# Kernel tuning notes

Hardware: AMD Instinct MI355X
Metric: run time of the kernel (lower is better)

Reference implementation:

```python
import jax, jax.numpy as jnp
import numpy as np

N_NODES = 10000
N_EDGES = 160000
F_DIM = 64
H = 4


def setup_inputs() -> dict:
    key = jax.random.key(0)
    ks = jax.random.split(key, 10)
    s = 1.0 / np.sqrt(F_DIM)  # xavier-ish scale
    return {
        "x": jax.random.normal(ks[0], (N_NODES, F_DIM), jnp.float32),
        "edge_index": jax.random.randint(ks[1], (2, N_EDGES), 0, N_NODES),
        "edge_vec": jax.random.normal(ks[2], (N_EDGES, 3), jnp.float32),
        "edge_len": jax.random.uniform(ks[3], (N_EDGES,), jnp.float32, 0.1, 5.0),
        "w_proj_W": jax.random.normal(ks[4], (H, F_DIM, F_DIM), jnp.float32) * s,
        "radial_W": jax.random.normal(ks[5], (H, F_DIM, F_DIM), jnp.float32) * s,
        "tangential_W": jax.random.normal(ks[6], (H, F_DIM, F_DIM), jnp.float32) * s,
        "radial_score": jax.random.normal(ks[7], (H, F_DIM), jnp.float32) * s,
        "tangential_score": jax.random.normal(ks[8], (H, F_DIM), jnp.float32) * s,
        "radial_distance_log_scale": jnp.zeros((), jnp.float32),
        "radial_temp_bias": jnp.zeros((H,), jnp.float32),
        "radial_temp_weight": jnp.zeros((H,), jnp.float32),
        "w_out_W": jax.random.normal(ks[9], (F_DIM, F_DIM), jnp.float32) * s,
    }


def _segment_softmax(logits, receiver, num_nodes):
    # logits: [E, H]; softmax over all edges sharing the same receiver.
    # Equivalent to the original's degree-bucketed per-group softmax.
    m = jax.ops.segment_max(logits, receiver, num_segments=num_nodes)  # [N, H]
    a = jnp.exp(logits - m[receiver])
    d = jax.ops.segment_sum(a, receiver, num_segments=num_nodes)       # [N, H]
    return a / d[receiver]


def reference(x, edge_index, edge_vec, edge_len, w_proj_W, radial_W, tangential_W,
              radial_score, tangential_score, radial_distance_log_scale,
              radial_temp_bias, radial_temp_weight, w_out_W):
    sender, receiver = edge_index[0], edge_index[1]
    n = x.shape[0]

    # Per-head bias-free linear projections (o3.Linear on scalar irreps).
    energy = jnp.einsum('nf,hfg->hng', x, w_proj_W)       # [H, N, F]
    radial = jnp.einsum('nf,hfg->hng', x, radial_W)       # [H, N, F]
    tang = jnp.einsum('nf,hfg->hng', x, tangential_W)     # [H, N, F]

    e_d = energy[:, sender] - energy[:, receiver]                       # [H, E, F]
    r_d = jnp.transpose(radial[:, sender] - radial[:, receiver], (1, 0, 2))  # [E, H, F]
    t_d = jnp.transpose(tang[:, sender] - tang[:, receiver], (1, 0, 2))      # [E, H, F]

    scale = jax.nn.softplus(radial_distance_log_scale)
    r_log = jnp.einsum('hef,hf->eh', e_d, radial_score) - scale * edge_len[:, None]  # [E, H]
    temp = jax.nn.softplus(radial_temp_bias[None, :] + radial_temp_weight[None, :] * edge_len[:, None])
    r_log = r_log / (temp + 0.0001)
    t_log = jnp.einsum('hef,hf->eh', e_d, tangential_score)                          # [E, H]

    r_alpha = _segment_softmax(r_log, receiver, n)  # [E, H]
    t_alpha = _segment_softmax(t_log, receiver, n)  # [E, H]

    r_msg = jax.ops.segment_sum(r_alpha[:, :, None] * r_d, receiver, num_segments=n)  # [N, H, F]
    t_msg = jax.ops.segment_sum(t_alpha[:, :, None] * t_d, receiver, num_segments=n)  # [N, H, F]

    out = jnp.nan_to_num((r_msg + t_msg).mean(axis=1))  # mean over heads -> [N, F]
    return x + out @ w_out_W
```

## Files before the change

kernel.cpp:

```cpp
#include <hip/hip_runtime.h>
#include <math.h>

#define N_NODES 10000
#define N_EDGES 160000
#define CAP 64

#define NB_SCORE 40
#define NB_BUCKET 625
#define NB_WPP 9
#define NB_D1 (NB_SCORE + NB_BUCKET + NB_WPP)

typedef short bf16x8 __attribute__((ext_vector_type(8)));
typedef float f32x4 __attribute__((ext_vector_type(4)));

__device__ __forceinline__ float bf2f(unsigned short u) {
    return __uint_as_float(((unsigned int)u) << 16);
}
__device__ __forceinline__ unsigned short f2bf(float f) {
    unsigned int x = __float_as_uint(f);
    unsigned int r = (x + 0x7fffu + ((x >> 16) & 1u)) >> 16;
    return (unsigned short)r;
}
__device__ __forceinline__ float softplus_f(float x) {
    return fmaxf(x, 0.f) + log1pf(expf(-fabsf(x)));
}

__global__ void __launch_bounds__(256) k_prep(const float* __restrict__ x,
                                              const float* __restrict__ wproj,
                                              const float* __restrict__ wrad,
                                              const float* __restrict__ wtan,
                                              const float* __restrict__ rsc,
                                              const float* __restrict__ tsc,
                                              const float* __restrict__ wout,
                                              const int* __restrict__ ei,
                                              const float* __restrict__ el,
                                              float* __restrict__ rs,
                                              float* __restrict__ ts,
                                              int* __restrict__ cur,
                                              int2* __restrict__ sbuf,
                                              unsigned short* __restrict__ wppT) {
    __shared__ __align__(16) float smem[8192];
    int b = blockIdx.x;
    int t = threadIdx.x;

    if (b < NB_SCORE) {
        float* vrl = smem;
        float* vtl = smem + 256;
        {
            int h = t >> 6, f = t & 63;
            const float* wrow = wproj + h * 4096 + f * 64;
            const float* rsp = rsc + h * 64;
            const float* tsp = tsc + h * 64;
            float ar = 0.f, at = 0.f;
            for (int g = 0; g < 64; ++g) {
                float w = wrow[g];
                ar += w * rsp[g];
                at += w * tsp[g];
            }
            vrl[t] = ar;
            vtl[t] = at;
        }
        __syncthreads();
        int n = b * 256 + t;
        if (n >= N_NODES) return;
        const float4* xr = (const float4*)(x + n * 64);
        float accr[4] = {0.f, 0.f, 0.f, 0.f};
        float acct[4] = {0.f, 0.f, 0.f, 0.f};
        for (int i = 0; i < 16; ++i) {
            float4 xv = xr[i];
#pragma unroll
            for (int h = 0; h < 4; ++h) {
                float4 a = ((const float4*)vrl)[h * 16 + i];
                accr[h] += xv.x * a.x + xv.y * a.y + xv.z * a.z + xv.w * a.w;
                float4 bb = ((const float4*)vtl)[h * 16 + i];
                acct[h] += xv.x * bb.x + xv.y * bb.y + xv.z * bb.z + xv.w * bb.w;
            }
        }
        ((float4*)rs)[n] = make_float4(accr[0], accr[1], accr[2], accr[3]);
        ((float4*)ts)[n] = make_float4(acct[0], acct[1], acct[2], acct[3]);
    } else if (b < NB_SCORE + NB_BUCKET) {
        int e = (b - NB_SCORE) * 256 + t;
        if (e >= N_EDGES) return;
        int s = ei[e];
        int r = ei[N_EDGES + e];
        float len = el[e];
        int pos = atomicAdd(&cur[r], 1);
        if (pos < CAP) sbuf[r * CAP + pos] = make_int2(s, __float_as_int(len));
    } else {
        int k = b - NB_SCORE - NB_BUCKET;
        float* wo = smem;
        float* am = smem + 4096;
        for (int i = 0; i < 16; ++i) wo[t + 256 * i] = wout[t + 256 * i];
        if (k < 8) {
            const float* M = (k < 4) ? (wrad + k * 4096) : (wtan + (k - 4) * 4096);
            for (int i = 0; i < 16; ++i) am[t + 256 * i] = M[t + 256 * i];
        } else {
            for (int i = 0; i < 16; ++i) {
                int e = t + 256 * i;
                float s = 0.f;
#pragma unroll
                for (int h = 0; h < 4; ++h) s += wrad[h * 4096 + e] + wtan[h * 4096 + e];
                am[e] = -s;
            }
        }
        __syncthreads();
        int c = t & 63;
        int fg = t >> 6;
        for (int j = 0; j < 16; ++j) {
            int f = fg * 16 + j;
            float acc = 0.f;
            for (int g = 0; g < 64; ++g) acc += am[f * 64 + g] * wo[g * 64 + c];
            wppT[c * 576 + k * 64 + f] = f2bf(acc * 0.25f);
        }
    }
}

__global__ void __launch_bounds__(256) k_node(const int* __restrict__ cur,
                                              const int2* __restrict__ sbuf,
                                              const float* __restrict__ rs,
                                              const float* __restrict__ ts,
                                              const float* __restrict__ rdls,
                                              const float* __restrict__ tb,
                                              const float* __restrict__ tw,
                                              const float* __restrict__ x,
                                              const unsigned short* __restrict__ wppT,
                                              float* __restrict__ out) {
    __shared__ __align__(16) unsigned short accL[16 * 584];
    __shared__ __align__(16) float aldsb[4][CAP * 8];
    __shared__ int sldsb[4][CAP];
    int t = threadIdx.x;
    int wid = t >> 6, lane = t & 63;
    int blk = blockIdx.x;

    float scale = softplus_f(rdls[0]);
    float tb0 = tb[0], tb1 = tb[1], tb2 = tb[2], tb3 = tb[3];
    float tw0 = tw[0], tw1 = tw[1], tw2 = tw[2], tw3 = tw[3];
    float* alds = aldsb[wid];
    int*   slds = sldsb[wid];

    for (int j = 0; j < 4; ++j) {
        int n = blk * 16 + wid * 4 + j;
        int row = wid * 4 + j;
        int deg = min(cur[n], CAP);

        float4 rsr = ((const float4*)rs)[n];
        float4 tsr = ((const float4*)ts)[n];

        const float NEG = -3.402823466e38f;
        float rl0 = NEG, rl1 = NEG, rl2 = NEG, rl3 = NEG;
        float tl0 = NEG, tl1 = NEG, tl2 = NEG, tl3 = NEG;
        int s_e = 0;
        if (lane < deg) {
            int2 sl = sbuf[n * CAP + lane];
            s_e = sl.x;
            float len = __int_as_float(sl.y);
            float4 rss = ((const float4*)rs)[s_e];
            float4 tss = ((const float4*)ts)[s_e];
            float sl0 = scale * len;
            float i0 = 1.f / (softplus_f(tb0 + tw0 * len) + 1e-4f);
            float i1 = 1.f / (softplus_f(tb1 + tw1 * len) + 1e-4f);
            float i2 = 1.f / (softplus_f(tb2 + tw2 * len) + 1e-4f);
            float i3 = 1.f / (softplus_f(tb3 + tw3 * len) + 1e-4f);
            rl0 = ((rss.x - rsr.x) - sl0) * i0;
            rl1 = ((rss.y - rsr.y) - sl0) * i1;
            rl2 = ((rss.z - rsr.z) - sl0) * i2;
            rl3 = ((rss.w - rsr.w) - sl0) * i3;
            tl0 = tss.x - tsr.x;
            tl1 = tss.y - tsr.y;
            tl2 = tss.z - tsr.z;
            tl3 = tss.w - tsr.w;
        }
        float mr0 = rl0, mr1 = rl1, mr2 = rl2, mr3 = rl3;
        float mt0 = tl0, mt1 = tl1, mt2 = tl2, mt3 = tl3;
#pragma unroll
        for (int d = 32; d >= 1; d >>= 1) {
            mr0 = fmaxf(mr0, __shfl_xor(mr0, d)); mr1 = fmaxf(mr1, __shfl_xor(mr1, d));
            mr2 = fmaxf(mr2, __shfl_xor(mr2, d)); mr3 = fmaxf(mr3, __shfl_xor(mr3, d));
            mt0 = fmaxf(mt0, __shfl_xor(mt0, d)); mt1 = fmaxf(mt1, __shfl_xor(mt1, d));
            mt2 = fmaxf(mt2, __shfl_xor(mt2, d)); mt3 = fmaxf(mt3, __shfl_xor(mt3, d));
        }
        float er0 = 0.f, er1 = 0.f, er2 = 0.f, er3 = 0.f;
        float et0 = 0.f, et1 = 0.f, et2 = 0.f, et3 = 0.f;
        if (lane < deg) {
            er0 = expf(rl0 - mr0); er1 = expf(rl1 - mr1);
            er2 = expf(rl2 - mr2); er3 = expf(rl3 - mr3);
            et0 = expf(tl0 - mt0); et1 = expf(tl1 - mt1);
            et2 = expf(tl2 - mt2); et3 = expf(tl3 - mt3);
        }
        float sr0 = er0, sr1 = er1, sr2 = er2, sr3 = er3;
        float st0 = et0, st1 = et1, st2 = et2, st3 = et3;
#pragma unroll
        for (int d = 32; d >= 1; d >>= 1) {
            sr0 += __shfl_xor(sr0, d); sr1 += __shfl_xor(sr1, d);
            sr2 += __shfl_xor(sr2, d); sr3 += __shfl_xor(sr3, d);
            st0 += __shfl_xor(st0, d); st1 += __shfl_xor(st1, d);
            st2 += __shfl_xor(st2, d); st3 += __shfl_xor(st3, d);
        }
        if (lane < deg) {
            float* ap = alds + lane * 8;
            ((float4*)ap)[0] = make_float4(er0 / sr0, er1 / sr1, er2 / sr2, er3 / sr3);
            ((float4*)ap)[1] = make_float4(et0 / st0, et1 / st1, et2 / st2, et3 / st3);
            slds[lane] = s_e;
        }

        float a0 = 0.f, a1 = 0.f, a2 = 0.f, a3 = 0.f;
        float b0 = 0.f, b1 = 0.f, b2 = 0.f, b3 = 0.f;
        int i = 0;
        for (; i + 2 <= deg; i += 2) {
            int s0 = slds[i], s1 = slds[i + 1];
            float4 ar0 = ((const float4*)(alds + i * 8))[0];
            float4 at0 = ((const float4*)(alds + i * 8))[1];
            float4 ar1 = ((const float4*)(alds + (i + 1) * 8))[0];
            float4 at1 = ((const float4*)(alds + (i + 1) * 8))[1];
            float xv0 = x[s0 * 64 + lane];
            float xv1 = x[s1 * 64 + lane];
            a0 += ar0.x * xv0 + ar1.x * xv1;
            a1 += ar0.y * xv0 + ar1.y * xv1;
            a2 += ar0.z * xv0 + ar1.z * xv1;
            a3 += ar0.w * xv0 + ar1.w * xv1;
            b0 += at0.x * xv0 + at1.x * xv1;
            b1 += at0.y * xv0 + at1.y * xv1;
            b2 += at0.z * xv0 + at1.z * xv1;
            b3 += at0.w * xv0 + at1.w * xv1;
        }
        if (i < deg) {
            int s0 = slds[i];
            float4 ar0 = ((const float4*)(alds + i * 8))[0];
            float4 at0 = ((const float4*)(alds + i * 8))[1];
            float xv0 = x[s0 * 64 + lane];
            a0 += ar0.x * xv0; a1 += ar0.y * xv0; a2 += ar0.z * xv0; a3 += ar0.w * xv0;
            b0 += at0.x * xv0; b1 += at0.y * xv0; b2 += at0.z * xv0; b3 += at0.w * xv0;
        }
        float c8 = (deg > 0) ? x[n * 64 + lane] : 0.f;

        unsigned short* arow = accL + row * 584;
        arow[0 * 64 + lane] = f2bf(a0);
        arow[1 * 64 + lane] = f2bf(a1);
        arow[2 * 64 + lane] = f2bf(a2);
        arow[3 * 64 + lane] = f2bf(a3);
        arow[4 * 64 + lane] = f2bf(b0);
        arow[5 * 64 + lane] = f2bf(b1);
        arow[6 * 64 + lane] = f2bf(b2);
        arow[7 * 64 + lane] = f2bf(b3);
        arow[8 * 64 + lane] = f2bf(c8);
    }
    __syncthreads();

    int c = lane & 15, q = lane >> 4;
    f32x4 dacc = {0.f, 0.f, 0.f, 0.f};
    const unsigned short* bp = wppT + (16 * wid + c) * 576 + q * 8;
    const unsigned short* ap = accL + c * 584 + q * 8;
#pragma unroll
    for (int kc = 0; kc < 18; ++kc) {
        bf16x8 af = *(const bf16x8*)(ap + kc * 32);
        bf16x8 bf = *(const bf16x8*)(bp + kc * 32);
        dacc = __builtin_amdgcn_mfma_f32_16x16x32_bf16(af, bf, dacc, 0, 0, 0);
    }
#pragma unroll
    for (int r = 0; r < 4; ++r) {
        int node = blk * 16 + q * 4 + r;
        int col = 16 * wid + c;
        out[node * 64 + col] = x[node * 64 + col] + dacc[r];
    }
}

extern "C" void kernel_launch(void* const* d_in, const int* in_sizes, int n_in,
                              void* d_out, int out_size, void* d_ws, size_t ws_size,
                              hipStream_t stream) {
    const float* x     = (const float*)d_in[0];
    const int*   ei    = (const int*)d_in[1];
    const float* el    = (const float*)d_in[3];
    const float* wproj = (const float*)d_in[4];
    const float* wrad  = (const float*)d_in[5];
    const float* wtan  = (const float*)d_in[6];
    const float* rsc   = (const float*)d_in[7];
    const float* tsc   = (const float*)d_in[8];
    const float* rdls  = (const float*)d_in[9];
    const float* tb    = (const float*)d_in[10];
    const float* tw    = (const float*)d_in[11];
    const float* wout  = (const float*)d_in[12];
    float* out = (float*)d_out;

    char* w = (char*)d_ws;
    size_t o = 0;
    auto nxt = [&](size_t bytes) -> char* {
        char* p = w + o;
        o += (bytes + 255) & ~(size_t)255;
        return p;
    };
    float* rs = (float*)nxt((size_t)N_NODES * 4 * 4);
    float* ts = (float*)nxt((size_t)N_NODES * 4 * 4);
    int*   cur = (int*)nxt((size_t)N_NODES * 4);
    int2*  sbuf = (int2*)nxt((size_t)N_NODES * CAP * 8);
    unsigned short* wppT = (unsigned short*)nxt((size_t)64 * 576 * 2);

    hipMemsetAsync(cur, 0, (size_t)N_NODES * 4, stream);

    k_prep<<<NB_D1, 256, 0, stream>>>(x, wproj, wrad, wtan, rsc, tsc, wout,
                                      ei, el, rs, ts, cur, sbuf, wppT);
    k_node<<<625, 256, 0, stream>>>(cur, sbuf, rs, ts, rdls, tb, tw, x, wppT, out);
}
```

Before: 137.5 us.

## Assign one wavefront per node in k_node with 1024-thread blocks

The node kernel now launches 1024 threads per block so each of 16 wavefronts handles a single node, instead of 4 wavefronts looping over 4 nodes each. The per-node softmax and gather loops run in parallel across more waves, which exposes more memory-level parallelism for the irregular x gathers. The gather loop is also unrolled by 4 to issue more independent loads. The trade-off is that only 4 of 16 waves do the MFMA projection while the rest sit idle after the barrier, and the larger per-block LDS plus the launch-bounds hint (1024, 8) may limit occupancy or push the compiler toward register spills.

```diff
diff --git a/kernel.cpp b/kernel.cpp
--- a/kernel.cpp
+++ b/kernel.cpp
@@ -115,19 +115,19 @@
     }
 }
 
-__global__ void __launch_bounds__(256) k_node(const int* __restrict__ cur,
-                                              const int2* __restrict__ sbuf,
-                                              const float* __restrict__ rs,
-                                              const float* __restrict__ ts,
-                                              const float* __restrict__ rdls,
-                                              const float* __restrict__ tb,
-                                              const float* __restrict__ tw,
-                                              const float* __restrict__ x,
-                                              const unsigned short* __restrict__ wppT,
-                                              float* __restrict__ out) {
+__global__ void __launch_bounds__(1024, 8) k_node(const int* __restrict__ cur,
+                                                  const int2* __restrict__ sbuf,
+                                                  const float* __restrict__ rs,
+                                                  const float* __restrict__ ts,
+                                                  const float* __restrict__ rdls,
+                                                  const float* __restrict__ tb,
+                                                  const float* __restrict__ tw,
+                                                  const float* __restrict__ x,
+                                                  const unsigned short* __restrict__ wppT,
+                                                  float* __restrict__ out) {
     __shared__ __align__(16) unsigned short accL[16 * 584];
-    __shared__ __align__(16) float aldsb[4][CAP * 8];
-    __shared__ int sldsb[4][CAP];
+    __shared__ __align__(16) float aldsb[16][CAP * 8];
+    __shared__ int sldsb[16][CAP];
     int t = threadIdx.x;
     int wid = t >> 6, lane = t & 63;
     int blk = blockIdx.x;
@@ -138,129 +138,134 @@
     float* alds = aldsb[wid];
     int*   slds = sldsb[wid];
 
-    for (int j = 0; j < 4; ++j) {
-        int n = blk * 16 + wid * 4 + j;
-        int row = wid * 4 + j;
-        int deg = min(cur[n], CAP);
-
-        float4 rsr = ((const float4*)rs)[n];
-        float4 tsr = ((const float4*)ts)[n];
-
-        const float NEG = -3.402823466e38f;
-        float rl0 = NEG, rl1 = NEG, rl2 = NEG, rl3 = NEG;
-        float tl0 = NEG, tl1 = NEG, tl2 = NEG, tl3 = NEG;
-        int s_e = 0;
-        if (lane < deg) {
-            int2 sl = sbuf[n * CAP + lane];
-            s_e = sl.x;
-            float len = __int_as_float(sl.y);
-            float4 rss = ((const float4*)rs)[s_e];
-            float4 tss = ((const float4*)ts)[s_e];
-            float sl0 = scale * len;
-            float i0 = 1.f / (softplus_f(tb0 + tw0 * len) + 1e-4f);
-            float i1 = 1.f / (softplus_f(tb1 + tw1 * len) + 1e-4f);
-            float i2 = 1.f / (softplus_f(tb2 + tw2 * len) + 1e-4f);
-            float i3 = 1.f / (softplus_f(tb3 + tw3 * len) + 1e-4f);
-            rl0 = ((rss.x - rsr.x) - sl0) * i0;
-            rl1 = ((rss.y - rsr.y) - sl0) * i1;
-            rl2 = ((rss.z - rsr.z) - sl0) * i2;
-            rl3 = ((rss.w - rsr.w) - sl0) * i3;
-            tl0 = tss.x - tsr.x;
-            tl1 = tss.y - tsr.y;
-            tl2 = tss.z - tsr.z;
-            tl3 = tss.w - tsr.w;
-        }
-        float mr0 = rl0, mr1 = rl1, mr2 = rl2, mr3 = rl3;
-        float mt0 = tl0, mt1 = tl1, mt2 = tl2, mt3 = tl3;
-#pragma unroll
-        for (int d = 32; d >= 1; d >>= 1) {
-            mr0 = fmaxf(mr0, __shfl_xor(mr0, d)); mr1 = fmaxf(mr1, __shfl_xor(mr1, d));
-            mr2 = fmaxf(mr2, __shfl_xor(mr2, d)); mr3 = fmaxf(mr3, __shfl_xor(mr3, d));
-            mt0 = fmaxf(mt0, __shfl_xor(mt0, d)); mt1 = fmaxf(mt1, __shfl_xor(mt1, d));
-            mt2 = fmaxf(mt2, __shfl_xor(mt2, d)); mt3 = fmaxf(mt3, __shfl_xor(mt3, d));
-        }
-        float er0 = 0.f, er1 = 0.f, er2 = 0.f, er3 = 0.f;
-        float et0 = 0.f, et1 = 0.f, et2 = 0.f, et3 = 0.f;
-        if (lane < deg) {
-            er0 = expf(rl0 - mr0); er1 = expf(rl1 - mr1);
-            er2 = expf(rl2 - mr2); er3 = expf(rl3 - mr3);
-            et0 = expf(tl0 - mt0); et1 = expf(tl1 - mt1);
-            et2 = expf(tl2 - mt2); et3 = expf(tl3 - mt3);
-        }
-        float sr0 = er0, sr1 = er1, sr2 = er2, sr3 = er3;
-        float st0 = et0, st1 = et1, st2 = et2, st3 = et3;
-#pragma unroll
-        for (int d = 32; d >= 1; d >>= 1) {
-            sr0 += __shfl_xor(sr0, d); sr1 += __shfl_xor(sr1, d);
-            sr2 += __shfl_xor(sr2, d); sr3 += __shfl_xor(sr3, d);
-            st0 += __shfl_xor(st0, d); st1 += __shfl_xor(st1, d);
-            st2 += __shfl_xor(st2, d); st3 += __shfl_xor(st3, d);
-        }
-        if (lane < deg) {
-            float* ap = alds + lane * 8;
-            ((float4*)ap)[0] = make_float4(er0 / sr0, er1 / sr1, er2 / sr2, er3 / sr3);
-            ((float4*)ap)[1] = make_float4(et0 / st0, et1 / st1, et2 / st2, et3 / st3);
-            slds[lane] = s_e;
-        }
-
-        float a0 = 0.f, a1 = 0.f, a2 = 0.f, a3 = 0.f;
-        float b0 = 0.f, b1 = 0.f, b2 = 0.f, b3 = 0.f;
-        int i = 0;
-        for (; i + 2 <= deg; i += 2) {
-            int s0 = slds[i], s1 = slds[i + 1];
-            float4 ar0 = ((const float4*)(alds + i * 8))[0];
-            float4 at0 = ((const float4*)(alds + i * 8))[1];
-            float4 ar1 = ((const float4*)(alds + (i + 1) * 8))[0];
-            float4 at1 = ((const float4*)(alds + (i + 1) * 8))[1];
-            float xv0 = x[s0 * 64 + lane];
-            float xv1 = x[s1 * 64 + lane];
-            a0 += ar0.x * xv0 + ar1.x * xv1;
-            a1 += ar0.y * xv0 + ar1.y * xv1;
-            a2 += ar0.z * xv0 + ar1.z * xv1;
-            a3 += ar0.w * xv0 + ar1.w * xv1;
-            b0 += at0.x * xv0 + at1.x * xv1;
-            b1 += at0.y * xv0 + at1.y * xv1;
-            b2 += at0.z * xv0 + at1.z * xv1;
-            b3 += at0.w * xv0 + at1.w * xv1;
-        }
-        if (i < deg) {
-            int s0 = slds[i];
-            float4 ar0 = ((const float4*)(alds + i * 8))[0];
-            float4 at0 = ((const float4*)(alds + i * 8))[1];
-            float xv0 = x[s0 * 64 + lane];
-            a0 += ar0.x * xv0; a1 += ar0.y * xv0; a2 += ar0.z * xv0; a3 += ar0.w * xv0;
-            b0 += at0.x * xv0; b1 += at0.y * xv0; b2 += at0.z * xv0; b3 += at0.w * xv0;
-        }
-        float c8 = (deg > 0) ? x[n * 64 + lane] : 0.f;
-
-        unsigned short* arow = accL + row * 584;
-        arow[0 * 64 + lane] = f2bf(a0);
-        arow[1 * 64 + lane] = f2bf(a1);
-        arow[2 * 64 + lane] = f2bf(a2);
-        arow[3 * 64 + lane] = f2bf(a3);
-        arow[4 * 64 + lane] = f2bf(b0);
-        arow[5 * 64 + lane] = f2bf(b1);
-        arow[6 * 64 + lane] = f2bf(b2);
-        arow[7 * 64 + lane] = f2bf(b3);
-        arow[8 * 64 + lane] = f2bf(c8);
-    }
+    int n = blk * 16 + wid;
+    int deg = min(cur[n], CAP);
+
+    float4 rsr = ((const float4*)rs)[n];
+    float4 tsr = ((const float4*)ts)[n];
+
+    const float NEG = -3.402823466e38f;
+    float rl0 = NEG, rl1 = NEG, rl2 = NEG, rl3 = NEG;
+    float tl0 = NEG, tl1 = NEG, tl2 = NEG, tl3 = NEG;
+    int s_e = 0;
+    if (lane < deg) {
+        int2 sl = sbuf[n * CAP + lane];
+        s_e = sl.x;
+        float len = __int_as_float(sl.y);
+        float4 rss = ((const float4*)rs)[s_e];
+        float4 tss = ((const float4*)ts)[s_e];
+        float sl0 = scale * len;
+        float i0 = 1.f / (softplus_f(tb0 + tw0 * len) + 1e-4f);
+        float i1 = 1.f / (softplus_f(tb1 + tw1 * len) + 1e-4f);
+        float i2 = 1.f / (softplus_f(tb2 + tw2 * len) + 1e-4f);
+        float i3 = 1.f / (softplus_f(tb3 + tw3 * len) + 1e-4f);
+        rl0 = ((rss.x - rsr.x) - sl0) * i0;
+        rl1 = ((rss.y - rsr.y) - sl0) * i1;
+        rl2 = ((rss.z - rsr.z) - sl0) * i2;
+        rl3 = ((rss.w - rsr.w) - sl0) * i3;
+        tl0 = tss.x - tsr.x;
+        tl1 = tss.y - tsr.y;
+        tl2 = tss.z - tsr.z;
+        tl3 = tss.w - tsr.w;
+    }
+    float mr0 = rl0, mr1 = rl1, mr2 = rl2, mr3 = rl3;
+    float mt0 = tl0, mt1 = tl1, mt2 = tl2, mt3 = tl3;
+#pragma unroll
+    for (int d = 32; d >= 1; d >>= 1) {
+        mr0 = fmaxf(mr0, __shfl_xor(mr0, d)); mr1 = fmaxf(mr1, __shfl_xor(mr1, d));
+        mr2 = fmaxf(mr2, __shfl_xor(mr2, d)); mr3 = fmaxf(mr3, __shfl_xor(mr3, d));
+        mt0 = fmaxf(mt0, __shfl_xor(mt0, d)); mt1 = fmaxf(mt1, __shfl_xor(mt1, d));
+        mt2 = fmaxf(mt2, __shfl_xor(mt2, d)); mt3 = fmaxf(mt3, __shfl_xor(mt3, d));
+    }
+    float er0 = 0.f, er1 = 0.f, er2 = 0.f, er3 = 0.f;
+    float et0 = 0.f, et1 = 0.f, et2 = 0.f, et3 = 0.f;
+    if (lane < deg) {
+        er0 = expf(rl0 - mr0); er1 = expf(rl1 - mr1);
+        er2 = expf(rl2 - mr2); er3 = expf(rl3 - mr3);
+        et0 = expf(tl0 - mt0); et1 = expf(tl1 - mt1);
+        et2 = expf(tl2 - mt2); et3 = expf(tl3 - mt3);
+    }
+    float sr0 = er0, sr1 = er1, sr2 = er2, sr3 = er3;
+    float st0 = et0, st1 = et1, st2 = et2, st3 = et3;
+#pragma unroll
+    for (int d = 32; d >= 1; d >>= 1) {
+        sr0 += __shfl_xor(sr0, d); sr1 += __shfl_xor(sr1, d);
+        sr2 += __shfl_xor(sr2, d); sr3 += __shfl_xor(sr3, d);
+        st0 += __shfl_xor(st0, d); st1 += __shfl_xor(st1, d);
+        st2 += __shfl_xor(st2, d); st3 += __shfl_xor(st3, d);
+    }
+    if (lane < deg) {
+        float* ap = alds + lane * 8;
+        ((float4*)ap)[0] = make_float4(er0 / sr0, er1 / sr1, er2 / sr2, er3 / sr3);
+        ((float4*)ap)[1] = make_float4(et0 / st0, et1 / st1, et2 / st2, et3 / st3);
+        slds[lane] = s_e;
+    }
+
+    float a0 = 0.f, a1 = 0.f, a2 = 0.f, a3 = 0.f;
+    float b0 = 0.f, b1 = 0.f, b2 = 0.f, b3 = 0.f;
+    int i = 0;
+    for (; i + 4 <= deg; i += 4) {
+        int s0 = slds[i], s1 = slds[i + 1], s2 = slds[i + 2], s3 = slds[i + 3];
+        float xv0 = x[s0 * 64 + lane];
+        float xv1 = x[s1 * 64 + lane];
+        float xv2 = x[s2 * 64 + lane];
+        float xv3 = x[s3 * 64 + lane];
+        float4 ar0 = ((const float4*)(alds + i * 8))[0];
+        float4 at0 = ((const float4*)(alds + i * 8))[1];
+        float4 ar1 = ((const float4*)(alds + (i + 1) * 8))[0];
+        float4 at1 = ((const float4*)(alds + (i + 1) * 8))[1];
+        float4 ar2 = ((const float4*)(alds + (i + 2) * 8))[0];
+        float4 at2 = ((const float4*)(alds + (i + 2) * 8))[1];
+        float4 ar3 = ((const float4*)(alds + (i + 3) * 8))[0];
+        float4 at3 = ((const float4*)(alds + (i + 3) * 8))[1];
+        a0 += ar0.x * xv0 + ar1.x * xv1 + ar2.x * xv2 + ar3.x * xv3;
+        a1 += ar0.y * xv0 + ar1.y * xv1 + ar2.y * xv2 + ar3.y * xv3;
+        a2 += ar0.z * xv0 + ar1.z * xv1 + ar2.z * xv2 + ar3.z * xv3;
+        a3 += ar0.w * xv0 + ar1.w * xv1 + ar2.w * xv2 + ar3.w * xv3;
+        b0 += at0.x * xv0 + at1.x * xv1 + at2.x * xv2 + at3.x * xv3;
+        b1 += at0.y * xv0 + at1.y * xv1 + at2.y * xv2 + at3.y * xv3;
+        b2 += at0.z * xv0 + at1.z * xv1 + at2.z * xv2 + at3.z * xv3;
+        b3 += at0.w * xv0 + at1.w * xv1 + at2.w * xv2 + at3.w * xv3;
+    }
+    for (; i < deg; ++i) {
+        int s0 = slds[i];
+        float xv0 = x[s0 * 64 + lane];
+        float4 ar0 = ((const float4*)(alds + i * 8))[0];
+        float4 at0 = ((const float4*)(alds + i * 8))[1];
+        a0 += ar0.x * xv0; a1 += ar0.y * xv0; a2 += ar0.z * xv0; a3 += ar0.w * xv0;
+        b0 += at0.x * xv0; b1 += at0.y * xv0; b2 += at0.z * xv0; b3 += at0.w * xv0;
+    }
+    float c8 = (deg > 0) ? x[n * 64 + lane] : 0.f;
+
+    unsigned short* arow = accL + wid * 584;
+    arow[0 * 64 + lane] = f2bf(a0);
+    arow[1 * 64 + lane] = f2bf(a1);
+    arow[2 * 64 + lane] = f2bf(a2);
+    arow[3 * 64 + lane] = f2bf(a3);
+    arow[4 * 64 + lane] = f2bf(b0);
+    arow[5 * 64 + lane] = f2bf(b1);
+    arow[6 * 64 + lane] = f2bf(b2);
+    arow[7 * 64 + lane] = f2bf(b3);
+    arow[8 * 64 + lane] = f2bf(c8);
     __syncthreads();
 
-    int c = lane & 15, q = lane >> 4;
-    f32x4 dacc = {0.f, 0.f, 0.f, 0.f};
-    const unsigned short* bp = wppT + (16 * wid + c) * 576 + q * 8;
-    const unsigned short* ap = accL + c * 584 + q * 8;
-#pragma unroll
-    for (int kc = 0; kc < 18; ++kc) {
-        bf16x8 af = *(const bf16x8*)(ap + kc * 32);
-        bf16x8 bf = *(const bf16x8*)(bp + kc * 32);
-        dacc = __builtin_amdgcn_mfma_f32_16x16x32_bf16(af, bf, dacc, 0, 0, 0);
-    }
-#pragma unroll
-    for (int r = 0; r < 4; ++r) {
-        int node = blk * 16 + q * 4 + r;
-        int col = 16 * wid + c;
-        out[node * 64 + col] = x[node * 64 + col] + dacc[r];
+    if (wid < 4) {
+        int c = lane & 15, q = lane >> 4;
+        f32x4 dacc = {0.f, 0.f, 0.f, 0.f};
+        const unsigned short* bp = wppT + (16 * wid + c) * 576 + q * 8;
+        const unsigned short* ap = accL + c * 584 + q * 8;
+#pragma unroll
+        for (int kc = 0; kc < 18; ++kc) {
+            bf16x8 af = *(const bf16x8*)(ap + kc * 32);
+            bf16x8 bf = *(const bf16x8*)(bp + kc * 32);
+            dacc = __builtin_amdgcn_mfma_f32_16x16x32_bf16(af, bf, dacc, 0, 0, 0);
+        }
+#pragma unroll
+        for (int r = 0; r < 4; ++r) {
+            int node = blk * 16 + q * 4 + r;
+            int col = 16 * wid + c;
+            out[node * 64 + col] = x[node * 64 + col] + dacc[r];
+        }
     }
 }
 
@@ -298,5 +303,5 @@
 
     k_prep<<<NB_D1, 256, 0, stream>>>(x, wproj, wrad, wtan, rsc, tsc, wout,
                                       ei, el, rs, ts, cur, sbuf, wppT);
-    k_node<<<625, 256, 0, stream>>>(cur, sbuf, rs, ts, rdls, tb, tw, x, wppT, out);
-}
+    k_node<<<625, 1024, 0, stream>>>(cur, sbuf, rs, ts, rdls, tb, tw, x, wppT, out);
+}
```

Result: faster. 127.1 us (-7.5%).
